# Performance work log

Hardware: AMD Instinct MI355X
Metric: run time of the kernel (lower is better)

The kernel has to match this reference:

```python
import jax, jax.numpy as jnp
import numpy as np

DIM = 64
N_ENTITY = 100000
N_RELATION = 32
N_LAYER = 2
B = 4096
T = 32


def setup_inputs() -> dict:
    key = jax.random.key(0)
    ks = jax.random.split(key, 16)
    inp = {
        'users': jax.random.randint(ks[0], (B,), 0, 50000),
        'items': jax.random.randint(ks[1], (B,), 0, 20000),
        'user_h': jax.random.randint(ks[2], (N_LAYER, B, T), 0, N_ENTITY),
        'user_r': jax.random.randint(ks[3], (N_LAYER, B, T), 0, N_RELATION),
        'user_t': jax.random.randint(ks[4], (N_LAYER, B, T), 0, N_ENTITY),
        'item_h': jax.random.randint(ks[5], (N_LAYER, B, T), 0, N_ENTITY),
        'item_r': jax.random.randint(ks[6], (N_LAYER, B, T), 0, N_RELATION),
        'item_t': jax.random.randint(ks[7], (N_LAYER, B, T), 0, N_ENTITY),
        # learned params (xavier-ish scale), stored [in, out] for clean matmuls
        'ent_emb': jax.random.normal(ks[8], (N_ENTITY, DIM), jnp.float32) * 0.05,
        'rel_emb': jax.random.normal(ks[9], (N_RELATION, DIM), jnp.float32) * 0.05,
        'att_w1': jax.random.normal(ks[10], (2 * DIM, DIM), jnp.float32) * 0.1,
        'att_w2': jax.random.normal(ks[11], (DIM, DIM), jnp.float32) * 0.1,
        'att_w3': jax.random.normal(ks[12], (DIM, 1), jnp.float32) * 0.1,
        'gate_w1': jax.random.normal(ks[13], (2 * DIM, DIM), jnp.float32) * 0.1,
        'gate_w2': jax.random.normal(ks[14], (DIM, DIM), jnp.float32) * 0.1,
    }
    return inp


def _knowledge_attention(h_e, r_e, t_e, att_w1, att_w2, att_w3, gate_w1, gate_w2):
    # h_e/r_e/t_e: [L, B, T, D]
    x = jnp.concatenate([h_e, r_e], axis=-1)                      # [L,B,T,2D]
    s = jax.nn.relu(jnp.einsum('lbtk,kd->lbtd', x, att_w1))
    s = jax.nn.relu(jnp.einsum('lbtd,de->lbte', s, att_w2))
    s = jax.nn.sigmoid(jnp.einsum('lbtd,do->lbto', s, att_w3))[..., 0]  # [L,B,T]
    att = jax.nn.softmax(s, axis=-1)                              # softmax over neighbors
    gate = 2.0 * jax.nn.sigmoid(
        jnp.einsum('lbtd,de->lbte',
                   jax.nn.relu(jnp.einsum('lbtk,kd->lbtd', x, gate_w1)),
                   gate_w2))                                       # [L,B,T,D]
    return jnp.sum(att[..., None] * gate * t_e, axis=2)          # [L,B,D]


def reference(users, items, user_h, user_r, user_t, item_h, item_r, item_t,
              ent_emb, rel_emb, att_w1, att_w2, att_w3, gate_w1, gate_w2):
    # ---- user tower ----
    u_h = ent_emb[user_h]   # [L,B,T,D]
    u_r = rel_emb[user_r]
    u_t = ent_emb[user_t]
    user_origin = jnp.mean(u_h[0], axis=1)                        # [B,D]
    u_layers = _knowledge_attention(u_h, u_r, u_t, att_w1, att_w2, att_w3,
                                    gate_w1, gate_w2)             # [L,B,D]
    e_u = jnp.concatenate([user_origin] + [u_layers[i] for i in range(N_LAYER)], axis=-1)
    # ---- item tower ----
    i_h = ent_emb[item_h]
    i_r = rel_emb[item_r]
    i_t = ent_emb[item_t]
    item_origin = ent_emb[items]                                  # [B,D]
    i_layers = _knowledge_attention(i_h, i_r, i_t, att_w1, att_w2, att_w3,
                                    gate_w1, gate_w2)
    e_v = jnp.concatenate([item_origin] + [i_layers[i] for i in range(N_LAYER)], axis=-1)
    # ---- predict (agg='concat', single concat block per tower) ----
    scores = jax.nn.sigmoid(jnp.sum(e_u * e_v, axis=1))           # [B]
    return scores
```

## Files before the change

### kernel.cpp

```cpp
#include <hip/hip_runtime.h>

#define DIM 64
#define NB 4096
#define NTOK 32
#define NL 2

typedef __attribute__((ext_vector_type(8))) __bf16 bf16x8;
typedef __attribute__((ext_vector_type(4))) float f32x4;

__device__ __forceinline__ f32x4 mfma16(bf16x8 a, bf16x8 b, f32x4 c) {
  return __builtin_amdgcn_mfma_f32_16x16x32_bf16(a, b, c, 0, 0, 0);
}

__global__ void prep_w(const float* __restrict__ W1, const float* __restrict__ G1,
                       const float* __restrict__ W2, const float* __restrict__ G2,
                       __bf16* __restrict__ ws) {
  int i = blockIdx.x * 256 + threadIdx.x;
  if (i < 8192) {
    int c = i >> 7, k = i & 127;
    ws[i]        = (__bf16)W1[k * 64 + c];
    ws[8192 + i] = (__bf16)G1[k * 64 + c];
  } else if (i < 12288) {
    int j = i - 8192;
    int c = j >> 6, k = j & 63;
    ws[16384 + j] = (__bf16)W2[k * 64 + c];
    ws[20480 + j] = (__bf16)G2[k * 64 + c];
  }
}

__global__ __launch_bounds__(256) void ckan_main(
    const int* __restrict__ items,
    const int* __restrict__ user_h, const int* __restrict__ user_r, const int* __restrict__ user_t,
    const int* __restrict__ item_h, const int* __restrict__ item_r, const int* __restrict__ item_t,
    const float* __restrict__ ent, const float* __restrict__ rel,
    const __bf16* __restrict__ wt, const float* __restrict__ w3,
    float* __restrict__ out)
{
  __shared__ __align__(16) __bf16 s1buf[128][72];
  __shared__ __align__(16) __bf16 g1buf[128][72];
  __shared__ float attbuf[128];
  __shared__ int hidx[128], ridx[128], tidx[128];

  const int tid  = threadIdx.x;
  const int w    = tid >> 6;
  const int lane = tid & 63;
  const int b    = blockIdx.x * 4 + w;
  const int r16  = lane & 15;
  const int g4   = lane >> 4;
  const int rb   = w * 32;

  const __bf16* __restrict__ W1t = wt;
  const __bf16* __restrict__ G1t = wt + 8192;
  const __bf16* __restrict__ W2t = wt + 16384;
  const __bf16* __restrict__ G2t = wt + 20480;

  const f32x4 zero4 = {0.f, 0.f, 0.f, 0.f};
  float layer_dot = 0.f;

  for (int l = 0; l < NL; ++l) {
    float uvec[4];
#pragma unroll
    for (int tower = 0; tower < 2; ++tower) {
      const int* __restrict__ Hp = tower ? item_h : user_h;
      const int* __restrict__ Rp = tower ? item_r : user_r;
      const int* __restrict__ Tp = tower ? item_t : user_t;
      const int ibase = (l * NB + b) * NTOK;
      if (lane < 32) {
        hidx[rb + lane] = Hp[ibase + lane];
        ridx[rb + lane] = Rp[ibase + lane];
        tidx[rb + lane] = Tp[ibase + lane];
      }

      const int h0 = hidx[rb + r16] * DIM;
      const int h1 = hidx[rb + 16 + r16] * DIM;
      const int rr0 = ridx[rb + r16] * DIM;
      const int rr1 = ridx[rb + 16 + r16] * DIM;

      f32x4 accS[2][4], accG[2][4];
#pragma unroll
      for (int m = 0; m < 2; ++m)
#pragma unroll
        for (int n = 0; n < 4; ++n) { accS[m][n] = zero4; accG[m][n] = zero4; }

#pragma unroll
      for (int kk = 0; kk < 4; ++kk) {
        bf16x8 afr[2];
#pragma unroll
        for (int m = 0; m < 2; ++m) {
          const float* src;
          if (kk < 2) src = ent + (m ? h1 : h0) + kk * 32 + g4 * 8;
          else        src = rel + (m ? rr1 : rr0) + (kk - 2) * 32 + g4 * 8;
          f32x4 lo = *(const f32x4*)(src);
          f32x4 hi = *(const f32x4*)(src + 4);
          bf16x8 a;
          a[0] = (__bf16)lo[0]; a[1] = (__bf16)lo[1]; a[2] = (__bf16)lo[2]; a[3] = (__bf16)lo[3];
          a[4] = (__bf16)hi[0]; a[5] = (__bf16)hi[1]; a[6] = (__bf16)hi[2]; a[7] = (__bf16)hi[3];
          afr[m] = a;
        }
#pragma unroll
        for (int n = 0; n < 4; ++n) {
          bf16x8 bS = *(const bf16x8*)(W1t + (n * 16 + r16) * 128 + kk * 32 + g4 * 8);
          bf16x8 bG = *(const bf16x8*)(G1t + (n * 16 + r16) * 128 + kk * 32 + g4 * 8);
#pragma unroll
          for (int m = 0; m < 2; ++m) {
            accS[m][n] = mfma16(afr[m], bS, accS[m][n]);
            accG[m][n] = mfma16(afr[m], bG, accG[m][n]);
          }
        }
      }

#pragma unroll
      for (int m = 0; m < 2; ++m)
#pragma unroll
        for (int n = 0; n < 4; ++n)
#pragma unroll
          for (int i = 0; i < 4; ++i) {
            const int row = rb + m * 16 + g4 * 4 + i;
            const int col = n * 16 + r16;
            s1buf[row][col] = (__bf16)fmaxf(accS[m][n][i], 0.f);
            g1buf[row][col] = (__bf16)fmaxf(accG[m][n][i], 0.f);
          }

      f32x4 acc2S[2][4], acc2G[2][4];
#pragma unroll
      for (int m = 0; m < 2; ++m)
#pragma unroll
        for (int n = 0; n < 4; ++n) { acc2S[m][n] = zero4; acc2G[m][n] = zero4; }
#pragma unroll
      for (int kk = 0; kk < 2; ++kk) {
        bf16x8 aS[2], aG[2];
#pragma unroll
        for (int m = 0; m < 2; ++m) {
          const int tok = rb + m * 16 + r16;
          aS[m] = *(const bf16x8*)&s1buf[tok][kk * 32 + g4 * 8];
          aG[m] = *(const bf16x8*)&g1buf[tok][kk * 32 + g4 * 8];
        }
#pragma unroll
        for (int n = 0; n < 4; ++n) {
          bf16x8 bS = *(const bf16x8*)(W2t + (n * 16 + r16) * 64 + kk * 32 + g4 * 8);
          bf16x8 bG = *(const bf16x8*)(G2t + (n * 16 + r16) * 64 + kk * 32 + g4 * 8);
#pragma unroll
          for (int m = 0; m < 2; ++m) {
            acc2S[m][n] = mfma16(aS[m], bS, acc2S[m][n]);
            acc2G[m][n] = mfma16(aG[m], bG, acc2G[m][n]);
          }
        }
      }

#pragma unroll
      for (int m = 0; m < 2; ++m)
#pragma unroll
        for (int n = 0; n < 4; ++n)
#pragma unroll
          for (int i = 0; i < 4; ++i)
            s1buf[rb + m * 16 + g4 * 4 + i][n * 16 + r16] = (__bf16)fmaxf(acc2S[m][n][i], 0.f);

      float sc = 0.f;
      if (lane < 32) {
        float dot = 0.f;
        const __bf16* srow = &s1buf[rb + lane][0];
#pragma unroll
        for (int c = 0; c < 64; ++c) dot += (float)srow[c] * w3[c];
        sc = 1.f / (1.f + __expf(-dot));
      }
      float mx = sc;
#pragma unroll
      for (int off = 16; off >= 1; off >>= 1) mx = fmaxf(mx, __shfl_xor(mx, off));
      float ex = __expf(sc - mx);
      float sm = ex;
#pragma unroll
      for (int off = 16; off >= 1; off >>= 1) sm += __shfl_xor(sm, off);
      if (lane < 32) attbuf[rb + lane] = ex / sm;

      float outn[4] = {0.f, 0.f, 0.f, 0.f};
#pragma unroll
      for (int m = 0; m < 2; ++m)
#pragma unroll
        for (int i = 0; i < 4; ++i) {
          const int trow = m * 16 + g4 * 4 + i;
          const float at = attbuf[rb + trow];
          const float* te = ent + tidx[rb + trow] * DIM;
#pragma unroll
          for (int n = 0; n < 4; ++n) {
            const float g2 = 2.f / (1.f + __expf(-acc2G[m][n][i]));
            outn[n] += at * g2 * te[n * 16 + r16];
          }
        }
#pragma unroll
      for (int n = 0; n < 4; ++n) {
        outn[n] += __shfl_xor(outn[n], 16);
        outn[n] += __shfl_xor(outn[n], 32);
      }
      if (tower == 0) {
#pragma unroll
        for (int n = 0; n < 4; ++n) uvec[n] = outn[n];
      } else {
#pragma unroll
        for (int n = 0; n < 4; ++n) layer_dot += uvec[n] * outn[n];
      }
    }
  }

  float uo = 0.f;
  const int ib0 = b * NTOK;
#pragma unroll 8
  for (int t = 0; t < NTOK; ++t) uo += ent[user_h[ib0 + t] * DIM + lane];
  uo *= (1.f / 32.f);
  const float io = ent[items[b] * DIM + lane];
  float part = uo * io + 0.25f * layer_dot;
#pragma unroll
  for (int off = 32; off >= 1; off >>= 1) part += __shfl_xor(part, off);
  if (lane == 0) out[b] = 1.f / (1.f + __expf(-part));
}

extern "C" void kernel_launch(void* const* d_in, const int* in_sizes, int n_in,
                              void* d_out, int out_size, void* d_ws, size_t ws_size,
                              hipStream_t stream) {
  const int*   items  = (const int*)d_in[1];
  const int*   user_h = (const int*)d_in[2];
  const int*   user_r = (const int*)d_in[3];
  const int*   user_t = (const int*)d_in[4];
  const int*   item_h = (const int*)d_in[5];
  const int*   item_r = (const int*)d_in[6];
  const int*   item_t = (const int*)d_in[7];
  const float* ent    = (const float*)d_in[8];
  const float* rel    = (const float*)d_in[9];
  const float* W1     = (const float*)d_in[10];
  const float* W2     = (const float*)d_in[11];
  const float* w3     = (const float*)d_in[12];
  const float* G1     = (const float*)d_in[13];
  const float* G2     = (const float*)d_in[14];
  __bf16* wt = (__bf16*)d_ws;
  float* out = (float*)d_out;

  prep_w<<<dim3(48), dim3(256), 0, stream>>>(W1, G1, W2, G2, wt);
  ckan_main<<<dim3(NB / 4), dim3(256), 0, stream>>>(
      items, user_h, user_r, user_t, item_h, item_r, item_t,
      ent, rel, wt, w3, out);
}
```

Baseline: 143.4 us.

## Pre-convert entity and relation tables to bf16 and compute attention in registers

Adds a prep kernel that converts the whole entity table, and the relation table, to bf16 in workspace each call. The main kernel then gathers head, relation and tail rows as bf16, halving bytes per random gather, with an fp32 fallback path when the workspace is too small. The attention score projection, sigmoid and softmax now run on the MFMA accumulators with lane shuffles instead of LDS round-trips, and indices are loaded straight from global memory. The trade is an extra full-table conversion pass per call, bf16 rounding of the tail embeddings, and a launch-bounds occupancy hint.

```diff
diff --git a/kernel.cpp b/kernel.cpp
--- a/kernel.cpp
+++ b/kernel.cpp
@@ -12,9 +12,15 @@
   return __builtin_amdgcn_mfma_f32_16x16x32_bf16(a, b, c, 0, 0, 0);
 }
 
+#define WT_OFF   0
+#define ENTB_OFF 24576
+#define RELB_OFF (24576 + 100000 * 64)
+#define WS_NEED_BYTES ((size_t)(RELB_OFF + 2048) * 2)
+
 __global__ void prep_w(const float* __restrict__ W1, const float* __restrict__ G1,
                        const float* __restrict__ W2, const float* __restrict__ G2,
-                       __bf16* __restrict__ ws) {
+                       const float* __restrict__ rel, __bf16* __restrict__ ws,
+                       int do_rel) {
   int i = blockIdx.x * 256 + threadIdx.x;
   if (i < 8192) {
     int c = i >> 7, k = i & 127;
@@ -25,21 +31,34 @@
     int c = j >> 6, k = j & 63;
     ws[16384 + j] = (__bf16)W2[k * 64 + c];
     ws[20480 + j] = (__bf16)G2[k * 64 + c];
+  } else if (do_rel && i < 14336) {
+    int j = i - 12288;
+    ws[RELB_OFF + j] = (__bf16)rel[j];
   }
 }
 
-__global__ __launch_bounds__(256) void ckan_main(
+__global__ void prep_ent(const float* __restrict__ ent, __bf16* __restrict__ entb) {
+  int t = blockIdx.x * 256 + threadIdx.x;
+  const float* src = ent + t * 8;
+  f32x4 lo = *(const f32x4*)src;
+  f32x4 hi = *(const f32x4*)(src + 4);
+  bf16x8 v;
+  v[0] = (__bf16)lo[0]; v[1] = (__bf16)lo[1]; v[2] = (__bf16)lo[2]; v[3] = (__bf16)lo[3];
+  v[4] = (__bf16)hi[0]; v[5] = (__bf16)hi[1]; v[6] = (__bf16)hi[2]; v[7] = (__bf16)hi[3];
+  *(bf16x8*)(entb + t * 8) = v;
+}
+
+template <bool BT>
+__global__ __launch_bounds__(256, 3) void ckan_main(
     const int* __restrict__ items,
     const int* __restrict__ user_h, const int* __restrict__ user_r, const int* __restrict__ user_t,
     const int* __restrict__ item_h, const int* __restrict__ item_r, const int* __restrict__ item_t,
     const float* __restrict__ ent, const float* __restrict__ rel,
-    const __bf16* __restrict__ wt, const float* __restrict__ w3,
+    const __bf16* __restrict__ wsb, const float* __restrict__ w3,
     float* __restrict__ out)
 {
   __shared__ __align__(16) __bf16 s1buf[128][72];
   __shared__ __align__(16) __bf16 g1buf[128][72];
-  __shared__ float attbuf[128];
-  __shared__ int hidx[128], ridx[128], tidx[128];
 
   const int tid  = threadIdx.x;
   const int w    = tid >> 6;
@@ -49,10 +68,16 @@
   const int g4   = lane >> 4;
   const int rb   = w * 32;
 
-  const __bf16* __restrict__ W1t = wt;
-  const __bf16* __restrict__ G1t = wt + 8192;
-  const __bf16* __restrict__ W2t = wt + 16384;
-  const __bf16* __restrict__ G2t = wt + 20480;
+  const __bf16* __restrict__ W1t = wsb;
+  const __bf16* __restrict__ G1t = wsb + 8192;
+  const __bf16* __restrict__ W2t = wsb + 16384;
+  const __bf16* __restrict__ G2t = wsb + 20480;
+  const __bf16* __restrict__ entb = wsb + ENTB_OFF;
+  const __bf16* __restrict__ relb = wsb + RELB_OFF;
+
+  float w3c[4];
+#pragma unroll
+  for (int n = 0; n < 4; ++n) w3c[n] = w3[n * 16 + r16];
 
   const f32x4 zero4 = {0.f, 0.f, 0.f, 0.f};
   float layer_dot = 0.f;
@@ -65,16 +90,17 @@
       const int* __restrict__ Rp = tower ? item_r : user_r;
       const int* __restrict__ Tp = tower ? item_t : user_t;
       const int ibase = (l * NB + b) * NTOK;
-      if (lane < 32) {
-        hidx[rb + lane] = Hp[ibase + lane];
-        ridx[rb + lane] = Rp[ibase + lane];
-        tidx[rb + lane] = Tp[ibase + lane];
-      }
-
-      const int h0 = hidx[rb + r16] * DIM;
-      const int h1 = hidx[rb + 16 + r16] * DIM;
-      const int rr0 = ridx[rb + r16] * DIM;
-      const int rr1 = ridx[rb + 16 + r16] * DIM;
+
+      const int h0  = Hp[ibase + r16] * DIM;
+      const int h1  = Hp[ibase + 16 + r16] * DIM;
+      const int rr0 = Rp[ibase + r16] * DIM;
+      const int rr1 = Rp[ibase + 16 + r16] * DIM;
+      int tof[2][4];
+#pragma unroll
+      for (int m = 0; m < 2; ++m)
+#pragma unroll
+        for (int i = 0; i < 4; ++i)
+          tof[m][i] = Tp[ibase + m * 16 + g4 * 4 + i] * DIM;
 
       f32x4 accS[2][4], accG[2][4];
 #pragma unroll
@@ -87,15 +113,22 @@
         bf16x8 afr[2];
 #pragma unroll
         for (int m = 0; m < 2; ++m) {
-          const float* src;
-          if (kk < 2) src = ent + (m ? h1 : h0) + kk * 32 + g4 * 8;
-          else        src = rel + (m ? rr1 : rr0) + (kk - 2) * 32 + g4 * 8;
-          f32x4 lo = *(const f32x4*)(src);
-          f32x4 hi = *(const f32x4*)(src + 4);
-          bf16x8 a;
-          a[0] = (__bf16)lo[0]; a[1] = (__bf16)lo[1]; a[2] = (__bf16)lo[2]; a[3] = (__bf16)lo[3];
-          a[4] = (__bf16)hi[0]; a[5] = (__bf16)hi[1]; a[6] = (__bf16)hi[2]; a[7] = (__bf16)hi[3];
-          afr[m] = a;
+          if (BT) {
+            const __bf16* src = (kk < 2)
+                ? entb + (m ? h1 : h0) + kk * 32 + g4 * 8
+                : relb + (m ? rr1 : rr0) + (kk - 2) * 32 + g4 * 8;
+            afr[m] = *(const bf16x8*)src;
+          } else {
+            const float* src = (kk < 2)
+                ? ent + (m ? h1 : h0) + kk * 32 + g4 * 8
+                : rel + (m ? rr1 : rr0) + (kk - 2) * 32 + g4 * 8;
+            f32x4 lo = *(const f32x4*)(src);
+            f32x4 hi = *(const f32x4*)(src + 4);
+            bf16x8 a;
+            a[0] = (__bf16)lo[0]; a[1] = (__bf16)lo[1]; a[2] = (__bf16)lo[2]; a[3] = (__bf16)lo[3];
+            a[4] = (__bf16)hi[0]; a[5] = (__bf16)hi[1]; a[6] = (__bf16)hi[2]; a[7] = (__bf16)hi[3];
+            afr[m] = a;
+          }
         }
 #pragma unroll
         for (int n = 0; n < 4; ++n) {
@@ -147,43 +180,66 @@
         }
       }
 
-#pragma unroll
-      for (int m = 0; m < 2; ++m)
-#pragma unroll
-        for (int n = 0; n < 4; ++n)
-#pragma unroll
-          for (int i = 0; i < 4; ++i)
-            s1buf[rb + m * 16 + g4 * 4 + i][n * 16 + r16] = (__bf16)fmaxf(acc2S[m][n][i], 0.f);
-
-      float sc = 0.f;
-      if (lane < 32) {
-        float dot = 0.f;
-        const __bf16* srow = &s1buf[rb + lane][0];
-#pragma unroll
-        for (int c = 0; c < 64; ++c) dot += (float)srow[c] * w3[c];
-        sc = 1.f / (1.f + __expf(-dot));
-      }
-      float mx = sc;
-#pragma unroll
-      for (int off = 16; off >= 1; off >>= 1) mx = fmaxf(mx, __shfl_xor(mx, off));
-      float ex = __expf(sc - mx);
-      float sm = ex;
-#pragma unroll
-      for (int off = 16; off >= 1; off >>= 1) sm += __shfl_xor(sm, off);
-      if (lane < 32) attbuf[rb + lane] = ex / sm;
+      float att[2][4];
+      {
+        float dotp[2][4];
+#pragma unroll
+        for (int m = 0; m < 2; ++m)
+#pragma unroll
+          for (int i = 0; i < 4; ++i) {
+            float d = 0.f;
+#pragma unroll
+            for (int n = 0; n < 4; ++n)
+              d += fmaxf(acc2S[m][n][i], 0.f) * w3c[n];
+            dotp[m][i] = d;
+          }
+#pragma unroll
+        for (int off = 1; off <= 8; off <<= 1)
+#pragma unroll
+          for (int m = 0; m < 2; ++m)
+#pragma unroll
+            for (int i = 0; i < 4; ++i)
+              dotp[m][i] += __shfl_xor(dotp[m][i], off);
+        float mx = -1.f;
+#pragma unroll
+        for (int m = 0; m < 2; ++m)
+#pragma unroll
+          for (int i = 0; i < 4; ++i) {
+            dotp[m][i] = 1.f / (1.f + __expf(-dotp[m][i]));
+            mx = fmaxf(mx, dotp[m][i]);
+          }
+        mx = fmaxf(mx, __shfl_xor(mx, 16));
+        mx = fmaxf(mx, __shfl_xor(mx, 32));
+        float sm = 0.f;
+#pragma unroll
+        for (int m = 0; m < 2; ++m)
+#pragma unroll
+          for (int i = 0; i < 4; ++i) {
+            att[m][i] = __expf(dotp[m][i] - mx);
+            sm += att[m][i];
+          }
+        sm += __shfl_xor(sm, 16);
+        sm += __shfl_xor(sm, 32);
+        const float inv = 1.f / sm;
+#pragma unroll
+        for (int m = 0; m < 2; ++m)
+#pragma unroll
+          for (int i = 0; i < 4; ++i) att[m][i] *= inv;
+      }
 
       float outn[4] = {0.f, 0.f, 0.f, 0.f};
 #pragma unroll
       for (int m = 0; m < 2; ++m)
 #pragma unroll
         for (int i = 0; i < 4; ++i) {
-          const int trow = m * 16 + g4 * 4 + i;
-          const float at = attbuf[rb + trow];
-          const float* te = ent + tidx[rb + trow] * DIM;
+          const float at = att[m][i];
+          const int to = tof[m][i];
 #pragma unroll
           for (int n = 0; n < 4; ++n) {
             const float g2 = 2.f / (1.f + __expf(-acc2G[m][n][i]));
-            outn[n] += at * g2 * te[n * 16 + r16];
+            const float te = BT ? (float)entb[to + n * 16 + r16]
+                                : ent[to + n * 16 + r16];
+            outn[n] += at * g2 * te;
           }
         }
 #pragma unroll
@@ -230,11 +286,19 @@
   const float* w3     = (const float*)d_in[12];
   const float* G1     = (const float*)d_in[13];
   const float* G2     = (const float*)d_in[14];
-  __bf16* wt = (__bf16*)d_ws;
+  __bf16* wsb = (__bf16*)d_ws;
   float* out = (float*)d_out;
 
-  prep_w<<<dim3(48), dim3(256), 0, stream>>>(W1, G1, W2, G2, wt);
-  ckan_main<<<dim3(NB / 4), dim3(256), 0, stream>>>(
-      items, user_h, user_r, user_t, item_h, item_r, item_t,
-      ent, rel, wt, w3, out);
-}
+  const bool bt = ws_size >= WS_NEED_BYTES;
+  prep_w<<<dim3(56), dim3(256), 0, stream>>>(W1, G1, W2, G2, rel, wsb, bt ? 1 : 0);
+  if (bt) {
+    prep_ent<<<dim3(3125), dim3(256), 0, stream>>>(ent, wsb + ENTB_OFF);
+    ckan_main<true><<<dim3(NB / 4), dim3(256), 0, stream>>>(
+        items, user_h, user_r, user_t, item_h, item_r, item_t,
+        ent, rel, wsb, w3, out);
+  } else {
+    ckan_main<false><<<dim3(NB / 4), dim3(256), 0, stream>>>(
+        items, user_h, user_r, user_t, item_h, item_r, item_t,
+        ent, rel, wsb, w3, out);
+  }
+}
```

After: 361.9 us. 152% more time.
